# Performance work log

Hardware: AMD Instinct MI355X
Metric: run time of the kernel (lower is better)

Reference implementation:

```python
import jax, jax.numpy as jnp
import numpy as np

B, IN_DIM, HID, K, D = 16384, 1024, 2048, 8192, 128
COMMIT = 0.25


def setup_inputs() -> dict:
    key = jax.random.key(0)
    ks = jax.random.split(key, 10)
    s1 = 1.0 / np.sqrt(IN_DIM)
    s2 = 1.0 / np.sqrt(HID)
    s3 = 1.0 / np.sqrt(D)
    return {
        "x": jax.random.uniform(ks[0], (B, IN_DIM), dtype=jnp.float32),
        "W1": jax.random.normal(ks[1], (IN_DIM, HID), dtype=jnp.float32) * s1,
        "b1": jnp.zeros((HID,), jnp.float32),
        "W2": jax.random.normal(ks[2], (HID, D), dtype=jnp.float32) * s2,
        "b2": jnp.zeros((D,), jnp.float32),
        # torch init: uniform(-1/K, 1/K)
        "codebook": jax.random.uniform(ks[3], (K, D), dtype=jnp.float32, minval=-1.0 / K, maxval=1.0 / K),
        "W3": jax.random.normal(ks[4], (D, HID), dtype=jnp.float32) * s3,
        "b3": jnp.zeros((HID,), jnp.float32),
        "W4": jax.random.normal(ks[5], (HID, IN_DIM), dtype=jnp.float32) * s2,
        "b4": jnp.zeros((IN_DIM,), jnp.float32),
    }


def reference(x, W1, b1, W2, b2, codebook, W3, b3, W4, b4):
    # Encoder MLP: [B, IN] -> [B, D]
    h = jax.nn.relu(x @ W1 + b1)
    z = h @ W2 + b2                                   # [B, D]

    # Squared-distance to codebook: ||z||^2 - 2 z C^T + ||C||^2  -> [B, K]
    dists = (jnp.sum(z * z, axis=1, keepdims=True)
             - 2.0 * (z @ codebook.T)
             + jnp.sum(codebook * codebook, axis=1))
    indices = jnp.argmin(dists, axis=1)               # [B]
    z_q = codebook[indices]                            # [B, D]

    # Straight-through estimator
    z_q_st = z + jax.lax.stop_gradient(z_q - z)

    # Decoder MLP: [B, D] -> [B, IN]
    h2 = jax.nn.relu(z_q_st @ W3 + b3)
    recon = jax.nn.sigmoid(h2 @ W4 + b4)

    sg_zq = jax.lax.stop_gradient(z_q)
    mse = jnp.mean(jnp.square(sg_zq - z))
    loss = mse + COMMIT * mse
    return (recon, loss, indices)
```

## Files before the change

### kernel.cpp

```cpp
#include <hip/hip_runtime.h>
#include <hip/hip_bf16.h>


#define B_    16384
#define INDIM 1024
#define HID   2048
#define KCB   8192
#define DDIM  128

#define CAND_CAP 2000000u
#define LBUF_CAP 1024u

typedef __bf16    bf16x8   __attribute__((ext_vector_type(8)));
typedef float     floatx4  __attribute__((ext_vector_type(4)));
typedef double    doublex4 __attribute__((ext_vector_type(4)));
typedef _Float16  half8    __attribute__((ext_vector_type(8)));
typedef __fp16    fp16x2   __attribute__((ext_vector_type(2)));

#define XS 4096.0f
#define WS 8192.0f
#define SCALE_INV 2.9802322387695312e-08

__device__ __forceinline__ unsigned long long pack_key(float d, int code)
{
    unsigned int u = __float_as_uint(d);
    u = (u & 0x80000000u) ? ~u : (u | 0x80000000u);
    return ((unsigned long long)u << 32) | (unsigned int)code;
}

__device__ __forceinline__ unsigned packf(float d)
{
    unsigned u = __float_as_uint(d);
    return (u & 0x80000000u) ? ~u : (u | 0x80000000u);
}
__device__ __forceinline__ float unpackf(unsigned p)
{
    unsigned u = (p & 0x80000000u) ? (p ^ 0x80000000u) : ~p;
    return __uint_as_float(u);
}

__device__ __forceinline__ void gll16(const float* g, float* l)
{
    __builtin_amdgcn_global_load_lds(
        (const __attribute__((address_space(1))) void*)g,
        (__attribute__((address_space(3))) void*)l, 16, 0, 0);
}

template <int ACT, int PMASK>
__launch_bounds__(256)
__global__ void gemm_split_f16(const float* __restrict__ A, const _Float16* __restrict__ Bs_g,
                               const float* __restrict__ bias, float* __restrict__ Cout,
                               int M, int N, int K)
{
    __shared__ float    As[128 * 32];
    __shared__ _Float16 Bsh[64 * 64];

    const int t    = threadIdx.x;
    const int m0   = blockIdx.y * 128, n0 = blockIdx.x * 64;
    const int wave = t >> 6, lane = t & 63;
    const int wr   = (wave >> 1) * 64, wc = (wave & 1) * 32;
    const int quad = lane >> 4, l16 = lane & 15;
    const int lr   = lane >> 3;
    const int lcA  = ((lane & 7) ^ lr) * 4;
    const int slB  = lane & 7;
    const int lrB  = lane >> 3;

    floatx4  accf[4][2];
    doublex4 accd[4][2];
#pragma unroll
    for (int i = 0; i < 4; ++i)
#pragma unroll
        for (int j = 0; j < 2; ++j) {
            accf[i][j] = (floatx4){0.f, 0.f, 0.f, 0.f};
            accd[i][j] = (doublex4){0.0, 0.0, 0.0, 0.0};
        }

    const int NKT = K >> 5;
    for (int kt = 0; kt < NKT; ++kt) {
        const int k0 = kt << 5;
        __syncthreads();
#pragma unroll
        for (int s = 0; s < 4; ++s) {
            int r = wave * 32 + s * 8;
            gll16(A + (size_t)(m0 + r + lr) * K + k0 + lcA, &As[r * 32]);
        }
#pragma unroll
        for (int s = 0; s < 2; ++s) {
            int rb = wave * 16 + s * 8 + lrB;
            int ccs = slB ^ (lrB & 7);
            gll16((const float*)(Bs_g + (size_t)(n0 + rb) * (2 * K) + kt * 64 + ccs * 8),
                  (float*)&Bsh[(wave * 16 + s * 8) * 64]);
        }
        __syncthreads();

        half8 a1[4], a2[4];
#pragma unroll
        for (int i = 0; i < 4; ++i) {
            const int row = wr + i * 16 + l16;
            const int s0  = (2 * quad) ^ (row & 7);
            const int s1  = (2 * quad + 1) ^ (row & 7);
            floatx4 f0 = *(const floatx4*)&As[row * 32 + s0 * 4];
            floatx4 f1 = *(const floatx4*)&As[row * 32 + s1 * 4];
            union { half8 v; fp16x2 h[4]; } u1, u2;
            float sv[8];
#pragma unroll
            for (int q = 0; q < 4; ++q) sv[q] = f0[q] * XS;
#pragma unroll
            for (int q = 0; q < 4; ++q) sv[4 + q] = f1[q] * XS;
#pragma unroll
            for (int q = 0; q < 4; ++q) {
                fp16x2 hi = __builtin_amdgcn_cvt_pkrtz(sv[2 * q], sv[2 * q + 1]);
                u1.h[q] = hi;
                float r0 = sv[2 * q] - (float)hi[0];
                float r1 = sv[2 * q + 1] - (float)hi[1];
                u2.h[q] = __builtin_amdgcn_cvt_pkrtz(r0, r1);
            }
            a1[i] = u1.v; a2[i] = u2.v;
        }
        half8 b1[2], b2[2];
#pragma unroll
        for (int j = 0; j < 2; ++j) {
            const int row = wc + j * 16 + l16;
            b1[j] = *(const half8*)&Bsh[row * 64 + ((0 + quad) ^ (row & 7)) * 8];
            b2[j] = *(const half8*)&Bsh[row * 64 + ((4 + quad) ^ (row & 7)) * 8];
        }
#pragma unroll
        for (int i = 0; i < 4; ++i)
#pragma unroll
            for (int j = 0; j < 2; ++j)
                accf[i][j] = __builtin_amdgcn_mfma_f32_16x16x32_f16(a1[i], b1[j], accf[i][j], 0, 0, 0);
#pragma unroll
        for (int i = 0; i < 4; ++i)
#pragma unroll
            for (int j = 0; j < 2; ++j)
                accf[i][j] = __builtin_amdgcn_mfma_f32_16x16x32_f16(a1[i], b2[j], accf[i][j], 0, 0, 0);
#pragma unroll
        for (int i = 0; i < 4; ++i)
#pragma unroll
            for (int j = 0; j < 2; ++j)
                accf[i][j] = __builtin_amdgcn_mfma_f32_16x16x32_f16(a2[i], b1[j], accf[i][j], 0, 0, 0);

        if ((kt & PMASK) == PMASK) {
#pragma unroll
            for (int i = 0; i < 4; ++i)
#pragma unroll
                for (int j = 0; j < 2; ++j) {
#pragma unroll
                    for (int r = 0; r < 4; ++r)
                        accd[i][j][r] += (double)accf[i][j][r] * SCALE_INV;
                    accf[i][j] = (floatx4){0.f, 0.f, 0.f, 0.f};
                }
        }
    }
    if (NKT & PMASK) {
#pragma unroll
        for (int i = 0; i < 4; ++i)
#pragma unroll
            for (int j = 0; j < 2; ++j)
#pragma unroll
                for (int r = 0; r < 4; ++r)
                    accd[i][j][r] += (double)accf[i][j][r] * SCALE_INV;
    }

#pragma unroll
    for (int i = 0; i < 4; ++i)
#pragma unroll
        for (int j = 0; j < 2; ++j)
#pragma unroll
            for (int r = 0; r < 4; ++r) {
                int row = m0 + wr + i * 16 + quad * 4 + r;
                int col = n0 + wc + j * 16 + l16;
                float f = (float)(accd[i][j][r] + (double)bias[col]);
                if (ACT == 1) f = fmaxf(f, 0.f);
                Cout[(size_t)row * N + col] = f;
            }
}

template <int IM, int ACT, int PMASK, int SPLITOUT>
__launch_bounds__(256)
__global__ void gemm_split_pre(const _Float16* __restrict__ As_g, const _Float16* __restrict__ Bs_g,
                               const float* __restrict__ bias, void* __restrict__ Cp,
                               int M, int N, int K)
{
    __shared__ _Float16 Ash[IM * 32 * 64];
    __shared__ _Float16 Bsh[64 * 64];

    const int t    = threadIdx.x;
    const int nwg  = gridDim.x * gridDim.y;
    int lin = blockIdx.y * gridDim.x + blockIdx.x;
    lin = (lin & 7) * (nwg >> 3) + (lin >> 3);
    const int bx = lin % gridDim.x, by = lin / gridDim.x;
    const int m0   = by * (IM * 32), n0 = bx * 64;
    const int wave = t >> 6, lane = t & 63;
    const int wr   = (wave >> 1) * (IM * 16), wc = (wave & 1) * 32;
    const int quad = lane >> 4, l16 = lane & 15;
    const int slB  = lane & 7;
    const int lrB  = lane >> 3;
    const int ccs  = slB ^ (lrB & 7);

    floatx4  accf[IM][2];
    doublex4 accd[IM][2];
#pragma unroll
    for (int i = 0; i < IM; ++i)
#pragma unroll
        for (int j = 0; j < 2; ++j) {
            accf[i][j] = (floatx4){0.f, 0.f, 0.f, 0.f};
            accd[i][j] = (doublex4){0.0, 0.0, 0.0, 0.0};
        }

    const int NKT = K >> 5;
    for (int kt = 0; kt < NKT; ++kt) {
        __syncthreads();
#pragma unroll
        for (int s = 0; s < IM; ++s) {
            int ra = wave * (IM * 8) + s * 8 + lrB;
            gll16((const float*)(As_g + (size_t)(m0 + ra) * (2 * K) + kt * 64 + ccs * 8),
                  (float*)&Ash[(wave * (IM * 8) + s * 8) * 64]);
        }
#pragma unroll
        for (int s = 0; s < 2; ++s) {
            int rb = wave * 16 + s * 8 + lrB;
            gll16((const float*)(Bs_g + (size_t)(n0 + rb) * (2 * K) + kt * 64 + ccs * 8),
                  (float*)&Bsh[(wave * 16 + s * 8) * 64]);
        }
        __syncthreads();

        half8 a1[IM], a2[IM], b1[2], b2[2];
#pragma unroll
        for (int i = 0; i < IM; ++i) {
            const int row = wr + i * 16 + l16;
            a1[i] = *(const half8*)&Ash[row * 64 + ((0 + quad) ^ (row & 7)) * 8];
            a2[i] = *(const half8*)&Ash[row * 64 + ((4 + quad) ^ (row & 7)) * 8];
        }
#pragma unroll
        for (int j = 0; j < 2; ++j) {
            const int row = wc + j * 16 + l16;
            b1[j] = *(const half8*)&Bsh[row * 64 + ((0 + quad) ^ (row & 7)) * 8];
            b2[j] = *(const half8*)&Bsh[row * 64 + ((4 + quad) ^ (row & 7)) * 8];
        }
#pragma unroll
        for (int i = 0; i < IM; ++i)
#pragma unroll
            for (int j = 0; j < 2; ++j)
                accf[i][j] = __builtin_amdgcn_mfma_f32_16x16x32_f16(a1[i], b1[j], accf[i][j], 0, 0, 0);
#pragma unroll
        for (int i = 0; i < IM; ++i)
#pragma unroll
            for (int j = 0; j < 2; ++j)
                accf[i][j] = __builtin_amdgcn_mfma_f32_16x16x32_f16(a1[i], b2[j], accf[i][j], 0, 0, 0);
#pragma unroll
        for (int i = 0; i < IM; ++i)
#pragma unroll
            for (int j = 0; j < 2; ++j)
                accf[i][j] = __builtin_amdgcn_mfma_f32_16x16x32_f16(a2[i], b1[j], accf[i][j], 0, 0, 0);

        if ((kt & PMASK) == PMASK) {
#pragma unroll
            for (int i = 0; i < IM; ++i)
#pragma unroll
                for (int j = 0; j < 2; ++j) {
#pragma unroll
                    for (int r = 0; r < 4; ++r)
                        accd[i][j][r] += (double)accf[i][j][r] * SCALE_INV;
                    accf[i][j] = (floatx4){0.f, 0.f, 0.f, 0.f};
                }
        }
    }
    if (NKT & PMASK) {
#pragma unroll
        for (int i = 0; i < IM; ++i)
#pragma unroll
            for (int j = 0; j < 2; ++j)
#pragma unroll
                for (int r = 0; r < 4; ++r)
                    accd[i][j][r] += (double)accf[i][j][r] * SCALE_INV;
    }

#pragma unroll
    for (int i = 0; i < IM; ++i)
#pragma unroll
        for (int j = 0; j < 2; ++j)
#pragma unroll
            for (int r = 0; r < 4; ++r) {
                int row = m0 + wr + i * 16 + quad * 4 + r;
                int col = n0 + wc + j * 16 + l16;
                float f = (float)(accd[i][j][r] + (double)bias[col]);
                if (ACT == 1) f = fmaxf(f, 0.f);
                if (SPLITOUT == 1) {
                    float sv = f * XS;
                    _Float16 p0 = (_Float16)sv;
                    _Float16 p1 = (_Float16)(sv - (float)p0);
                    _Float16* hs = (_Float16*)Cp;
                    size_t base = (size_t)row * (2 * (size_t)N)
                                + (size_t)(col >> 5) * 64 + (col & 31);
                    hs[base]      = p0;
                    hs[base + 32] = p1;
                } else {
                    ((float*)Cp)[(size_t)row * N + col] = f;
                }
            }
}

template <int ACT>
__launch_bounds__(256)
__global__ void gemm_bf16_gll(const __bf16* __restrict__ A, const __bf16* __restrict__ BT,
                              const float* __restrict__ bias, void* __restrict__ Cp,
                              int M, int N, int K)
{
    __shared__ __bf16 Asm[128 * 32];
    __shared__ __bf16 Bsm[128 * 32];

    const int t    = threadIdx.x;
    const int nwg  = gridDim.x * gridDim.y;
    int lin = blockIdx.y * gridDim.x + blockIdx.x;
    lin = (lin & 7) * (nwg >> 3) + (lin >> 3);
    const int bx = lin % gridDim.x, by = lin / gridDim.x;
    const int m0   = by * 128, n0 = bx * 128;
    const int wave = t >> 6, lane = t & 63;
    const int wr   = (wave >> 1) * 64, wc = (wave & 1) * 64;
    const int quad = lane >> 4, l16 = lane & 15;
    const int srow = lane >> 2;
    const int schk = lane & 3;

    floatx4 acc[4][4];
#pragma unroll
    for (int i = 0; i < 4; ++i)
#pragma unroll
        for (int j = 0; j < 4; ++j) acc[i][j] = (floatx4){0.f, 0.f, 0.f, 0.f};

    for (int k0 = 0; k0 < K; k0 += 32) {
        __syncthreads();
#pragma unroll
        for (int s = 0; s < 2; ++s) {
            const int rbase = wave * 32 + s * 16;
            const int ra = rbase + srow;
            const int cs = (schk - (ra >> 1)) & 3;
            gll16((const float*)(A + (size_t)(m0 + ra) * K + k0 + cs * 8),
                  (float*)&Asm[rbase * 32]);
        }
#pragma unroll
        for (int s = 0; s < 2; ++s) {
            const int rbase = wave * 32 + s * 16;
            const int rb = rbase + srow;
            const int cs = (schk - (rb >> 1)) & 3;
            gll16((const float*)(BT + (size_t)(n0 + rb) * K + k0 + cs * 8),
                  (float*)&Bsm[rbase * 32]);
        }
        __syncthreads();

        bf16x8 af[4], bfr[4];
#pragma unroll
        for (int i = 0; i < 4; ++i) {
            const int rl = wr + i * 16 + l16;
            const int sl = (quad + (rl >> 1)) & 3;
            af[i] = *(const bf16x8*)&Asm[rl * 32 + sl * 8];
        }
#pragma unroll
        for (int j = 0; j < 4; ++j) {
            const int rl = wc + j * 16 + l16;
            const int sl = (quad + (rl >> 1)) & 3;
            bfr[j] = *(const bf16x8*)&Bsm[rl * 32 + sl * 8];
        }
#pragma unroll
        for (int i = 0; i < 4; ++i)
#pragma unroll
            for (int j = 0; j < 4; ++j)
                acc[i][j] = __builtin_amdgcn_mfma_f32_16x16x32_bf16(af[i], bfr[j], acc[i][j], 0, 0, 0);
    }

#pragma unroll
    for (int i = 0; i < 4; ++i)
#pragma unroll
        for (int j = 0; j < 4; ++j) {
            int col = n0 + wc + j * 16 + l16;
            float b = bias[col];
#pragma unroll
            for (int r = 0; r < 4; ++r) {
                int row = m0 + wr + i * 16 + quad * 4 + r;
                float v = acc[i][j][r] + b;
                if (ACT == 1) {
                    v = fmaxf(v, 0.f);
                    ((__bf16*)Cp)[(size_t)row * N + col] = (__bf16)v;
                } else {
                    v = 1.f / (1.f + __expf(-v));
                    ((float*)Cp)[(size_t)row * N + col] = v;
                }
            }
        }
}

__global__ void split_x(const float* __restrict__ in, _Float16* __restrict__ outS, int n8)
{
    int i = blockIdx.x * 256 + threadIdx.x;
    if (i >= n8) return;
    const int K = INDIM;
    int m  = i / (K / 8);
    int k8 = i % (K / 8);
    int k  = k8 * 8;
    const float* src = in + (size_t)m * K + k;
    floatx4 f0 = *(const floatx4*)(src);
    floatx4 f1 = *(const floatx4*)(src + 4);
    union { half8 v; fp16x2 h[4]; } u1, u2;
    float sv[8];
#pragma unroll
    for (int q = 0; q < 4; ++q) sv[q] = f0[q] * XS;
#pragma unroll
    for (int q = 0; q < 4; ++q) sv[4 + q] = f1[q] * XS;
#pragma unroll
    for (int q = 0; q < 4; ++q) {
        fp16x2 hi = __builtin_amdgcn_cvt_pkrtz(sv[2 * q], sv[2 * q + 1]);
        u1.h[q] = hi;
        float r0 = sv[2 * q] - (float)hi[0];
        float r1 = sv[2 * q + 1] - (float)hi[1];
        u2.h[q] = __builtin_amdgcn_cvt_pkrtz(r0, r1);
    }
    size_t base = (size_t)m * (2 * K) + (size_t)(k >> 5) * 64 + (k & 31);
    *(half8*)(outS + base)      = u1.v;
    *(half8*)(outS + base + 32) = u2.v;
}

__global__ void transpose_split_f16(const float* __restrict__ in, _Float16* __restrict__ outS,
                                    int K, int N)
{
    __shared__ float tile[32][33];
    int k0 = blockIdx.x * 32, n0 = blockIdx.y * 32;
    int tr = threadIdx.x >> 5, tc = threadIdx.x & 31;
#pragma unroll
    for (int s = 0; s < 4; ++s)
        tile[tr + 8 * s][tc] = in[(size_t)(k0 + tr + 8 * s) * N + n0 + tc];
    __syncthreads();
#pragma unroll
    for (int s = 0; s < 4; ++s) {
        int n = n0 + tr + 8 * s;
        int k = k0 + tc;
        float w = tile[tc][tr + 8 * s] * WS;
        _Float16 p0 = (_Float16)w;
        float r = w - (float)p0;
        _Float16 p1 = (_Float16)r;
        size_t base = (size_t)n * (2 * K) + (size_t)(k >> 5) * 64 + (k & 31);
        outS[base]      = p0;
        outS[base + 32] = p1;
    }
}

__global__ void rownorm_kernel(const float* __restrict__ M, float* __restrict__ nrm)
{
    int k = blockIdx.x * 4 + (threadIdx.x >> 6);
    int lane = threadIdx.x & 63;
    float2 c = *(const float2*)(M + (size_t)k * DDIM + lane * 2);
    float q0 = c.x * c.x;
    float q1 = c.y * c.y;
    double s = (double)q0 + (double)q1;
#pragma unroll
    for (int off = 32; off > 0; off >>= 1) s += __shfl_down(s, off);
    if (lane == 0) nrm[k] = (float)s;
}

__global__ void cnmax_kernel(const float* __restrict__ cn, float* __restrict__ out)
{
    __shared__ float red[4];
    int t = threadIdx.x;
    float m = 0.f;
    for (int i = t; i < KCB; i += 256) m = fmaxf(m, cn[i]);
#pragma unroll
    for (int off = 32; off > 0; off >>= 1) m = fmaxf(m, __shfl_down(m, off));
    if ((t & 63) == 0) red[t >> 6] = m;
    __syncthreads();
    if (t == 0) out[0] = fmaxf(fmaxf(red[0], red[1]), fmaxf(red[2], red[3]));
}

__global__ void cvt_half(const float* __restrict__ in, _Float16* __restrict__ out,
                         float scale, int n8)
{
    int i = blockIdx.x * 256 + threadIdx.x;
    if (i >= n8) return;
    const float4 a = *(const float4*)(in + (size_t)i * 8);
    const float4 b = *(const float4*)(in + (size_t)i * 8 + 4);
    half8 h;
    h[0] = (_Float16)(a.x * scale); h[1] = (_Float16)(a.y * scale);
    h[2] = (_Float16)(a.z * scale); h[3] = (_Float16)(a.w * scale);
    h[4] = (_Float16)(b.x * scale); h[5] = (_Float16)(b.y * scale);
    h[6] = (_Float16)(b.z * scale); h[7] = (_Float16)(b.w * scale);
    *(half8*)(out + (size_t)i * 8) = h;
}

__launch_bounds__(256)
__global__ void score_sweep3(const _Float16* __restrict__ zh, const _Float16* __restrict__ ch,
                             const float* __restrict__ nz32, const float* __restrict__ cn32,
                             const float* __restrict__ cnmaxp,
                             unsigned* __restrict__ listCnt, unsigned* __restrict__ list)
{
    __shared__ __align__(16) _Float16 Zs[32 * 128];
    __shared__ __align__(16) _Float16 Cs[128 * 128];
    __shared__ unsigned rowmin[32];
    __shared__ unsigned lbuf[LBUF_CAP];
    __shared__ unsigned lcnt, lbase;

    const int t    = threadIdx.x;
    int bid = blockIdx.x;
    bid = (bid & 7) * ((int)gridDim.x >> 3) + (bid >> 3);
    const int m0   = bid * 32;
    const int wave = t >> 6, lane = t & 63;
    const int quad = lane >> 4, l16 = lane & 15;
    const int srow = lane >> 4, sc = lane & 15;

    if (t == 0) lcnt = 0u;
    if (t < 32) rowmin[t] = 0xFFFFFFFFu;

#pragma unroll
    for (int s = 0; s < 2; ++s) {
        const int rbase = s * 16 + wave * 4;
        const int ra = rbase + srow;
        const int cs = sc ^ ((ra & 7) << 1);
        gll16((const float*)(zh + (size_t)(m0 + ra) * 128 + cs * 8),
              (float*)&Zs[rbase * 128]);
    }
    __syncthreads();

    half8 af[2][4];
#pragma unroll
    for (int i = 0; i < 2; ++i) {
        const int rl = i * 16 + l16;
#pragma unroll
        for (int ks = 0; ks < 4; ++ks) {
            const int cc = (ks * 4 + quad) ^ ((rl & 7) << 1);
            af[i][ks] = *(const half8*)&Zs[rl * 128 + cc * 8];
        }
    }

    const float cnm = *cnmaxp;
    float nzv[8], W[8];
    unsigned cachemin[8];
    int rowidx[8];
#pragma unroll
    for (int i = 0; i < 2; ++i)
#pragma unroll
        for (int r = 0; r < 4; ++r) {
            const int q = i * 4 + r;
            rowidx[q] = i * 16 + quad * 4 + r;
            const int grow = m0 + rowidx[q];
            nzv[q] = nz32[grow];
            W[q]   = 2.4e-3f * sqrtf(nzv[q] * cnm) + 6.0e-5f;
            cachemin[q] = 0xFFFFFFFFu;
        }

    for (int nt = 0; nt < KCB / 128; ++nt) {
        const int n0 = nt * 128;
        __syncthreads();
#pragma unroll
        for (int s = 0; s < 8; ++s) {
            const int rbase = s * 16 + wave * 4;
            const int ra = rbase + srow;
            const int cs = sc ^ ((ra & 7) << 1);
            gll16((const float*)(ch + (size_t)(n0 + ra) * 128 + cs * 8),
                  (float*)&Cs[rbase * 128]);
        }
        float cnj[2];
#pragma unroll
        for (int j = 0; j < 2; ++j)
            cnj[j] = cn32[n0 + wave * 32 + j * 16 + l16];
        __syncthreads();

        floatx4 acc[2][2];
#pragma unroll
        for (int i = 0; i < 2; ++i)
#pragma unroll
            for (int j = 0; j < 2; ++j) acc[i][j] = (floatx4){0.f, 0.f, 0.f, 0.f};
#pragma unroll
        for (int ks = 0; ks < 4; ++ks) {
            half8 bf[2];
#pragma unroll
            for (int j = 0; j < 2; ++j) {
                const int rl = wave * 32 + j * 16 + l16;
                const int cc = (ks * 4 + quad) ^ ((rl & 7) << 1);
                bf[j] = *(const half8*)&Cs[rl * 128 + cc * 8];
            }
#pragma unroll
            for (int i = 0; i < 2; ++i)
#pragma unroll
                for (int j = 0; j < 2; ++j)
                    acc[i][j] = __builtin_amdgcn_mfma_f32_16x16x32_f16(af[i][ks], bf[j], acc[i][j], 0, 0, 0);
        }

        float dv[8][2];
#pragma unroll
        for (int i = 0; i < 2; ++i)
#pragma unroll
            for (int r = 0; r < 4; ++r) {
                const int q = i * 4 + r;
#pragma unroll
                for (int j = 0; j < 2; ++j) {
                    float s = acc[i][j][r] * (1.0f / 4096.0f);
                    dv[q][j] = (nzv[q] - 2.0f * s) + cnj[j];
                }
                unsigned lp = packf(fminf(dv[q][0], dv[q][1]));
                if (lp < cachemin[q])
                    atomicMin(&rowmin[rowidx[q]], lp);
            }
        __syncthreads();

#pragma unroll
        for (int i = 0; i < 2; ++i)
#pragma unroll
            for (int r = 0; r < 4; ++r) {
                const int q = i * 4 + r;
                unsigned rp = rowmin[rowidx[q]];
                cachemin[q] = rp;
                const float thr = unpackf(rp) + W[q];
#pragma unroll
                for (int j = 0; j < 2; ++j) {
                    if (dv[q][j] <= thr) {
                        const int code = n0 + wave * 32 + j * 16 + l16;
                        unsigned ent = ((unsigned)(m0 + rowidx[q]) << 13) | (unsigned)code;
                        unsigned idx = atomicAdd(&lcnt, 1u);
                        if (idx < LBUF_CAP) lbuf[idx] = ent;
                        else {
                            unsigned g = atomicAdd(listCnt, 1u);
                            if (g < CAND_CAP) list[g] = ent;
                        }
                    }
                }
            }
    }

    __syncthreads();
    unsigned cnt = lcnt; if (cnt > LBUF_CAP) cnt = LBUF_CAP;
    if (t == 0) lbase = atomicAdd(listCnt, cnt);
    __syncthreads();
    for (unsigned e = t; e < cnt; e += 256) {
        unsigned g = lbase + e;
        if (g < CAND_CAP) list[g] = lbuf[e];
    }
}

__launch_bounds__(256)
__global__ void refine_kernel(const float* __restrict__ z, const float* __restrict__ cb,
                              const float* __restrict__ nz32, const float* __restrict__ cn32,
                              const unsigned* __restrict__ listCnt,
                              const unsigned* __restrict__ list,
                              unsigned long long* __restrict__ gbest)
{
    unsigned cnt = *listCnt;
    if (cnt > CAND_CAP) cnt = CAND_CAP;
    const int lane = threadIdx.x & 63;
    for (unsigned p = blockIdx.x * 4 + (threadIdx.x >> 6); p < cnt; p += gridDim.x * 4) {
        const unsigned e = list[p];
        const int r = (int)(e >> 13), k = (int)(e & 8191u);
        float2 zv = *(const float2*)(z  + (size_t)r * DDIM + lane * 2);
        float2 cv = *(const float2*)(cb + (size_t)k * DDIM + lane * 2);
        double s = (double)zv.x * (double)cv.x + (double)zv.y * (double)cv.y;
#pragma unroll
        for (int off = 32; off > 0; off >>= 1) s += __shfl_down(s, off);
        if (lane == 0) {
            float s32 = (float)s;
            float d = (nz32[r] - 2.0f * s32) + cn32[k];
            atomicMin(&gbest[r], pack_key(d, k));
        }
    }
}

__global__ void init_gbest(unsigned long long* __restrict__ g,
                           double* __restrict__ acc, unsigned* __restrict__ cnt)
{
    g[blockIdx.x * 256 + threadIdx.x] = ~0ull;
    if (blockIdx.x == 0 && threadIdx.x == 0) { *acc = 0.0; *cnt = 0u; }
}

__global__ void gather_zq_loss(const float* __restrict__ z, const float* __restrict__ cb,
                               const unsigned long long* __restrict__ gbest,
                               __bf16* __restrict__ zqb, double* __restrict__ acc)
{
    int r = blockIdx.x * 4 + (threadIdx.x >> 6);
    int lane = threadIdx.x & 63;
    int k = (int)(gbest[r] & 0xffffffffull);
    float2 zv = *(const float2*)(z  + (size_t)r * DDIM + lane * 2);
    float2 cv = *(const float2*)(cb + (size_t)k * DDIM + lane * 2);
    __bf16 b0 = (__bf16)cv.x, b1 = (__bf16)cv.y;
    zqb[(size_t)r * DDIM + lane * 2]     = b0;
    zqb[(size_t)r * DDIM + lane * 2 + 1] = b1;
    double dx = (double)cv.x - (double)zv.x, dy = (double)cv.y - (double)zv.y;
    double s = dx * dx + dy * dy;
#pragma unroll
    for (int off = 32; off > 0; off >>= 1) s += __shfl_down(s, off);
    if (lane == 0) atomicAdd(acc, s);
}

__global__ void finalize_kernel(const unsigned long long* __restrict__ gbest,
                                const double* __restrict__ acc, float* __restrict__ out)
{
    int tid = blockIdx.x * 256 + threadIdx.x;
    if (tid < B_) out[16777217 + tid] = (float)(int)(gbest[tid] & 0xffffffffull);
    if (tid == 0) out[16777216] = (float)((*acc) * 1.25 / (double)(B_ * DDIM));
}

__global__ void transpose_to_bf16(const float* __restrict__ in, __bf16* __restrict__ outT,
                                  int K, int N)
{
    __shared__ float tile[32][33];
    int k0 = blockIdx.x * 32, n0 = blockIdx.y * 32;
    int tr = threadIdx.x >> 5, tc = threadIdx.x & 31;
#pragma unroll
    for (int s = 0; s < 4; ++s)
        tile[tr + 8 * s][tc] = in[(size_t)(k0 + tr + 8 * s) * N + n0 + tc];
    __syncthreads();
#pragma unroll
    for (int s = 0; s < 4; ++s)
        outT[(size_t)(n0 + tr + 8 * s) * K + k0 + tc] = (__bf16)tile[tc][tr + 8 * s];
}

extern "C" void kernel_launch(void* const* d_in, const int* in_sizes, int n_in,
                              void* d_out, int out_size, void* d_ws, size_t ws_size,
                              hipStream_t stream)
{
    const float* x  = (const float*)d_in[0];
    const float* W1 = (const float*)d_in[1];
    const float* b1 = (const float*)d_in[2];
    const float* W2 = (const float*)d_in[3];
    const float* b2 = (const float*)d_in[4];
    const float* cb = (const float*)d_in[5];
    const float* W3 = (const float*)d_in[6];
    const float* b3 = (const float*)d_in[7];
    const float* W4 = (const float*)d_in[8];
    const float* b4 = (const float*)d_in[9];
    float* out = (float*)d_out;

    char* ws = (char*)d_ws;
    _Float16* hs = (_Float16*)(ws);
    float*  h    = (float*)(ws);
    __bf16* h2b  = (__bf16*)(ws + 16777216ull);
    _Float16* zh  = (_Float16*)(ws);
    _Float16* chh = (_Float16*)(ws + 4194304ull);
    unsigned* list = (unsigned*)(ws + 8388608ull);
    float*  z32  = (float*)(ws + 134217728ull);
    __bf16* zqb  = (__bf16*)(ws + 142606336ull);
    _Float16* W1s = (_Float16*)(ws + 142606336ull);
    float*  nz32 = (float*)(ws + 150994944ull);
    float*  cn32 = (float*)(ws + 151060480ull);
    unsigned long long* gbest = (unsigned long long*)(ws + 151093248ull);
    double* acc  = (double*)(ws + 151224320ull);
    float*  cnmax   = (float*)(ws + 151224328ull);
    unsigned* listCnt = (unsigned*)(ws + 151224332ull);
    __bf16* W3t  = (__bf16*)(ws + 151228416ull);
    __bf16* W4t  = (__bf16*)(ws + 151752704ull);
    _Float16* W2s = (_Float16*)(ws + 155947008ull);

    const unsigned long long XS_OFF = 157286400ull;
    _Float16* xs = (_Float16*)(ws + XS_OFF);
    const bool pre_split_x = (ws_size >= XS_OFF + 67108864ull);

    init_gbest<<<B_ / 256, 256, 0, stream>>>(gbest, acc, listCnt);
    rownorm_kernel<<<KCB / 4, 256, 0, stream>>>(cb, cn32);
    cnmax_kernel<<<1, 256, 0, stream>>>(cn32, cnmax);
    transpose_to_bf16<<<dim3(DDIM / 32, HID / 32), 256, 0, stream>>>(W3, W3t, DDIM, HID);
    transpose_to_bf16<<<dim3(HID / 32, INDIM / 32), 256, 0, stream>>>(W4, W4t, HID, INDIM);
    transpose_split_f16<<<dim3(INDIM / 32, HID / 32), 256, 0, stream>>>(W1, W1s, INDIM, HID);
    transpose_split_f16<<<dim3(HID / 32, DDIM / 32), 256, 0, stream>>>(W2, W2s, HID, DDIM);

    if (pre_split_x) {
        split_x<<<(B_ * INDIM / 8) / 256, 256, 0, stream>>>(x, xs, B_ * INDIM / 8);
        gemm_split_pre<4, 1, 3, 1><<<dim3(HID / 64, B_ / 128), 256, 0, stream>>>(
            xs, W1s, b1, (void*)hs, B_, HID, INDIM);
        gemm_split_pre<2, 0, 1, 0><<<dim3(DDIM / 64, B_ / 64), 256, 0, stream>>>(
            hs, W2s, b2, (void*)z32, B_, DDIM, HID);
    } else {
        gemm_split_f16<1, 3><<<dim3(HID / 64, B_ / 128), 256, 0, stream>>>(
            x, W1s, b1, h, B_, HID, INDIM);
        gemm_split_f16<0, 1><<<dim3(DDIM / 64, B_ / 128), 256, 0, stream>>>(
            h, W2s, b2, z32, B_, DDIM, HID);
    }
    rownorm_kernel<<<B_ / 4, 256, 0, stream>>>(z32, nz32);

    cvt_half<<<(B_ * DDIM / 8) / 256, 256, 0, stream>>>(z32, zh, 1.0f, B_ * DDIM / 8);
    cvt_half<<<(KCB * DDIM / 8) / 256, 256, 0, stream>>>(cb, chh, 4096.0f, KCB * DDIM / 8);
    score_sweep3<<<B_ / 32, 256, 0, stream>>>(
        zh, chh, nz32, cn32, cnmax, listCnt, list);
    refine_kernel<<<1024, 256, 0, stream>>>(z32, cb, nz32, cn32, listCnt, list, gbest);

    gather_zq_loss<<<B_ / 4, 256, 0, stream>>>(z32, cb, gbest, zqb, acc);
    gemm_bf16_gll<1><<<dim3(HID / 128, B_ / 128), 256, 0, stream>>>(
        zqb, W3t, b3, (void*)h2b, B_, HID, DDIM);
    gemm_bf16_gll<2><<<dim3(INDIM / 128, B_ / 128), 256, 0, stream>>>(
        h2b, W4t, b4, (void*)out, B_, INDIM, HID);

    finalize_kernel<<<B_ / 256, 256, 0, stream>>>(gbest, acc, out);
}
```

Baseline: 947.1 us.

## Double-buffer LDS tiles in GEMM kernels to overlap loads with MFMA

Both the split-fp16 GEMM and the bf16 GEMM now use two LDS buffers for their A and B tiles. The next K-tile's global-to-LDS loads are issued before the MFMAs on the current tile, and each iteration needs one barrier instead of two. The aim is to hide global load latency behind matrix-core work and cut barrier overhead. The cost is twice the LDS per block, which may lower occupancy. Correctness relies on the barrier also waiting for the outstanding async LDS loads.

```diff
diff --git a/kernel.cpp b/kernel.cpp
--- a/kernel.cpp
+++ b/kernel.cpp
@@ -182,8 +182,8 @@
                                const float* __restrict__ bias, void* __restrict__ Cp,
                                int M, int N, int K)
 {
-    __shared__ _Float16 Ash[IM * 32 * 64];
-    __shared__ _Float16 Bsh[64 * 64];
+    __shared__ _Float16 Ash[2][IM * 32 * 64];
+    __shared__ _Float16 Bsh[2][64 * 64];
 
     const int t    = threadIdx.x;
     const int nwg  = gridDim.x * gridDim.y;
@@ -208,35 +208,41 @@
             accd[i][j] = (doublex4){0.0, 0.0, 0.0, 0.0};
         }
 
-    const int NKT = K >> 5;
-    for (int kt = 0; kt < NKT; ++kt) {
-        __syncthreads();
+    auto stage = [&](int kt, int b) {
 #pragma unroll
         for (int s = 0; s < IM; ++s) {
             int ra = wave * (IM * 8) + s * 8 + lrB;
             gll16((const float*)(As_g + (size_t)(m0 + ra) * (2 * K) + kt * 64 + ccs * 8),
-                  (float*)&Ash[(wave * (IM * 8) + s * 8) * 64]);
+                  (float*)&Ash[b][(wave * (IM * 8) + s * 8) * 64]);
         }
 #pragma unroll
         for (int s = 0; s < 2; ++s) {
             int rb = wave * 16 + s * 8 + lrB;
             gll16((const float*)(Bs_g + (size_t)(n0 + rb) * (2 * K) + kt * 64 + ccs * 8),
-                  (float*)&Bsh[(wave * 16 + s * 8) * 64]);
-        }
-        __syncthreads();
+                  (float*)&Bsh[b][(wave * 16 + s * 8) * 64]);
+        }
+    };
+
+    const int NKT = K >> 5;
+    stage(0, 0);
+    __syncthreads();
+
+    for (int kt = 0; kt < NKT; ++kt) {
+        const int cur = kt & 1;
+        if (kt + 1 < NKT) stage(kt + 1, cur ^ 1);
 
         half8 a1[IM], a2[IM], b1[2], b2[2];
 #pragma unroll
         for (int i = 0; i < IM; ++i) {
             const int row = wr + i * 16 + l16;
-            a1[i] = *(const half8*)&Ash[row * 64 + ((0 + quad) ^ (row & 7)) * 8];
-            a2[i] = *(const half8*)&Ash[row * 64 + ((4 + quad) ^ (row & 7)) * 8];
+            a1[i] = *(const half8*)&Ash[cur][row * 64 + ((0 + quad) ^ (row & 7)) * 8];
+            a2[i] = *(const half8*)&Ash[cur][row * 64 + ((4 + quad) ^ (row & 7)) * 8];
         }
 #pragma unroll
         for (int j = 0; j < 2; ++j) {
             const int row = wc + j * 16 + l16;
-            b1[j] = *(const half8*)&Bsh[row * 64 + ((0 + quad) ^ (row & 7)) * 8];
-            b2[j] = *(const half8*)&Bsh[row * 64 + ((4 + quad) ^ (row & 7)) * 8];
+            b1[j] = *(const half8*)&Bsh[cur][row * 64 + ((0 + quad) ^ (row & 7)) * 8];
+            b2[j] = *(const half8*)&Bsh[cur][row * 64 + ((4 + quad) ^ (row & 7)) * 8];
         }
 #pragma unroll
         for (int i = 0; i < IM; ++i)
@@ -265,6 +271,7 @@
                     accf[i][j] = (floatx4){0.f, 0.f, 0.f, 0.f};
                 }
         }
+        __syncthreads();
     }
     if (NKT & PMASK) {
 #pragma unroll
@@ -307,8 +314,8 @@
                               const float* __restrict__ bias, void* __restrict__ Cp,
                               int M, int N, int K)
 {
-    __shared__ __bf16 Asm[128 * 32];
-    __shared__ __bf16 Bsm[128 * 32];
+    __shared__ __bf16 Asm[2][128 * 32];
+    __shared__ __bf16 Bsm[2][128 * 32];
 
     const int t    = threadIdx.x;
     const int nwg  = gridDim.x * gridDim.y;
@@ -328,15 +335,14 @@
 #pragma unroll
         for (int j = 0; j < 4; ++j) acc[i][j] = (floatx4){0.f, 0.f, 0.f, 0.f};
 
-    for (int k0 = 0; k0 < K; k0 += 32) {
-        __syncthreads();
+    auto stage = [&](int k0, int b) {
 #pragma unroll
         for (int s = 0; s < 2; ++s) {
             const int rbase = wave * 32 + s * 16;
             const int ra = rbase + srow;
             const int cs = (schk - (ra >> 1)) & 3;
             gll16((const float*)(A + (size_t)(m0 + ra) * K + k0 + cs * 8),
-                  (float*)&Asm[rbase * 32]);
+                  (float*)&Asm[b][rbase * 32]);
         }
 #pragma unroll
         for (int s = 0; s < 2; ++s) {
@@ -344,28 +350,38 @@
             const int rb = rbase + srow;
             const int cs = (schk - (rb >> 1)) & 3;
             gll16((const float*)(BT + (size_t)(n0 + rb) * K + k0 + cs * 8),
-                  (float*)&Bsm[rbase * 32]);
-        }
-        __syncthreads();
+                  (float*)&Bsm[b][rbase * 32]);
+        }
+    };
+
+    const int NKT = K >> 5;
+    stage(0, 0);
+    __syncthreads();
+
+    for (int kt = 0; kt < NKT; ++kt) {
+        const int cur = kt & 1;
+        if (kt + 1 < NKT) stage((kt + 1) << 5, cur ^ 1);
 
         bf16x8 af[4], bfr[4];
 #pragma unroll
         for (int i = 0; i < 4; ++i) {
             const int rl = wr + i * 16 + l16;
             const int sl = (quad + (rl >> 1)) & 3;
-            af[i] = *(const bf16x8*)&Asm[rl * 32 + sl * 8];
+            af[i] = *(const bf16x8*)&Asm[cur][rl * 32 + sl * 8];
         }
 #pragma unroll
         for (int j = 0; j < 4; ++j) {
             const int rl = wc + j * 16 + l16;
             const int sl = (quad + (rl >> 1)) & 3;
-            bfr[j] = *(const bf16x8*)&Bsm[rl * 32 + sl * 8];
+            bfr[j] = *(const bf16x8*)&Bsm[cur][rl * 32 + sl * 8];
         }
 #pragma unroll
         for (int i = 0; i < 4; ++i)
 #pragma unroll
             for (int j = 0; j < 4; ++j)
                 acc[i][j] = __builtin_amdgcn_mfma_f32_16x16x32_bf16(af[i], bfr[j], acc[i][j], 0, 0, 0);
+
+        __syncthreads();
     }
 
 #pragma unroll
```

Result: slower. 1.008 ms (+6.4%).
